# Optimization experiments

Measured on AMD Instinct MI355X. Metric: run time of the kernel, lower is better.

## Reference

```python
import jax, jax.numpy as jnp
import numpy as np

B, N, DIM, H, DH = 2, 2048, 512, 8, 64
INNER = H * DH  # == DIM, required by the q.view trick in the original module
STEP = 4


def setup_inputs() -> dict:
    key = jax.random.key(0)
    k1, k2, k3 = jax.random.split(key, 3)
    x = jax.random.normal(k1, (B, N, DIM), jnp.float32)
    # to_qkv: Linear(dim, 4*inner_dim, bias=False); stored as [in, out] for x @ W
    W_qkv = jax.random.normal(k2, (DIM, 4 * INNER), jnp.float32) * 0.02
    # to_out: Linear(2*inner_dim, dim) with bias
    W_out = jax.random.normal(k3, (2 * INNER, DIM), jnp.float32) * 0.02
    b_out = jnp.zeros((DIM,), jnp.float32)
    return {"x": x, "W_qkv": W_qkv, "W_out": W_out, "b_out": b_out}


def reference(x, W_qkv, W_out, b_out):
    b, n, _ = x.shape
    h, dh = H, DH
    scale = dh ** -0.5

    qkvt = x @ W_qkv                       # [b, n, 4*inner]
    q, k, v, t = jnp.split(qkvt, 4, axis=-1)
    to_heads = lambda z: z.reshape(b, n, h, dh).transpose(0, 2, 1, 3)  # [b,h,n,dh]
    q, k, v, t = map(to_heads, (q, k, v, t))

    # pad q by repeating its last row yushu times (note: yushu=4 when n%4==0)
    yushu = STEP - n % STEP
    q = jnp.concatenate([q, jnp.repeat(q[:, :, -1:, :], yushu, axis=2)], axis=2)
    q0 = q.reshape(b, h, STEP, (n + yushu) // STEP, dh)[:, :, 0]  # [b,h,(n+yushu)/4,dh]
    q = jnp.tile(q0, (1, 1, STEP, 1))[:, :, :n]                   # [b,h,n,dh]

    dots = jnp.einsum('bhnd,bhmd->bhnm', q, k) * scale
    attn1 = jax.nn.softmax(dots, axis=-1)

    # fixed distance-decay attention: exp(-|i-j|/e), column-normalized
    pos = jnp.arange(1, n + 1, dtype=x.dtype)
    tg = jnp.abs(pos[None, :] - pos[:, None])                     # [n, n]
    attn2 = jnp.exp(-tg / jnp.exp(jnp.asarray(1.0, x.dtype)))
    # torch: attn2 / attn2.sum(-1) broadcasts [n] over last axis (divides column j by row-sum j)
    attn2 = attn2 / attn2.sum(-1)

    out1 = jnp.einsum('bhnm,bhmd->bhnd', attn1, v)
    out2 = jnp.einsum('nm,bhmd->bhnd', attn2, t)  # attn2 shared across b,h; no repeat needed
    out = jnp.concatenate([out1, out2], axis=-1)   # [b,h,n,2*dh]
    out = out.transpose(0, 2, 1, 3).reshape(b, n, 2 * h * dh)  # b n (h d)
    return out @ W_out + b_out  # dropout=0.0 -> identity
```

## Files before the change

### kernel.cpp

```cpp
#include <hip/hip_runtime.h>

#define NSEQ 2048
#define NB   2
#define NH   8

typedef unsigned short u16;
typedef __attribute__((ext_vector_type(8))) short s8v;
typedef __attribute__((ext_vector_type(4))) float f4v;

static __device__ __forceinline__ u16 f2bf(float f) {
  unsigned u = __float_as_uint(f);
  unsigned r = (u + 0x7fffu + ((u >> 16) & 1u)) >> 16;
  return (u16)r;
}
static __device__ __forceinline__ unsigned pk2(float a, float b) {
  return (unsigned)f2bf(a) | ((unsigned)f2bf(b) << 16);
}
static __device__ __forceinline__ float bf2f(u16 v) {
  return __uint_as_float(((unsigned)v) << 16);
}

typedef __attribute__((address_space(3))) unsigned int lds_u32;
typedef const __attribute__((address_space(1))) unsigned int glob_u32;
static __device__ __forceinline__ void load16(const void* g, void* l) {
  __builtin_amdgcn_global_load_lds((glob_u32*)g, (lds_u32*)l, 16, 0, 0);
}

__global__ __launch_bounds__(256)
void prep_kernel(const float* __restrict__ x, const float* __restrict__ Wqkv,
                 const float* __restrict__ Wout, u16* __restrict__ xb,
                 u16* __restrict__ WqkvT, u16* __restrict__ W1hi,
                 u16* __restrict__ W2hi) {
  __shared__ float tile[32][33];
  const int bid = blockIdx.x;
  if (bid < 1024) {
    long i = ((long)bid * 256 + threadIdx.x) * 8;
    float4 a = *(const float4*)&x[i];
    float4 b = *(const float4*)&x[i + 4];
    uint4 w;
    w.x = pk2(a.x, a.y); w.y = pk2(a.z, a.w);
    w.z = pk2(b.x, b.y); w.w = pk2(b.z, b.w);
    *(uint4*)&xb[i] = w;
    return;
  }
  const int tx = threadIdx.x & 31, ty = threadIdx.x >> 5;
  if (bid < 2048) {
    int b2 = bid - 1024;
    int c0 = (b2 & 63) * 32, r0 = (b2 >> 6) * 32;
#pragma unroll
    for (int s = 0; s < 32; s += 8)
      tile[ty + s][tx] = Wqkv[(long)(r0 + ty + s) * 2048 + c0 + tx];
    __syncthreads();
#pragma unroll
    for (int s = 0; s < 32; s += 8)
      WqkvT[(long)(c0 + ty + s) * 512 + r0 + tx] = f2bf(tile[tx][ty + s]);
    return;
  }
  {
    int b3 = bid - 2048;
    int part = b3 >= 256;
    if (part) b3 -= 256;
    u16* hi = part ? W2hi : W1hi;
    int c0 = (b3 & 15) * 32, r0 = (b3 >> 4) * 32;
#pragma unroll
    for (int s = 0; s < 32; s += 8) {
      int k = r0 + ty + s;
      int srcrow = ((k >> 6) * 128) + part * 64 + (k & 63);
      tile[ty + s][tx] = Wout[(long)srcrow * 512 + c0 + tx];
    }
    __syncthreads();
#pragma unroll
    for (int s = 0; s < 32; s += 8) {
      long o = (long)(c0 + ty + s) * 512 + r0 + tx;
      hi[o] = f2bf(tile[tx][ty + s]);
    }
  }
}

__global__ __launch_bounds__(256)
void gemm1_fused(const u16* __restrict__ xb, const u16* __restrict__ WqkvT,
                 u16* __restrict__ qkvtb, u16* __restrict__ qu,
                 u16* __restrict__ VtG) {
  const int bx = blockIdx.x, by = blockIdx.y;
  const bool isq = bx >= 12;
  if (isq && by >= 9) return;
  __shared__ alignas(16) u16 As[128 * 32];
  __shared__ alignas(16) u16 Bs[128 * 32];
  const int tid = threadIdx.x, lane = tid & 63, wave = tid >> 6;
  const int l15 = lane & 15, quad = lane >> 4;
  const int wr = wave >> 1, wc = wave & 1;
  const int Brow0 = isq ? (bx - 12) * 128 : 512 + bx * 128;

  f4v acc[4][4];
#pragma unroll
  for (int i = 0; i < 4; ++i)
#pragma unroll
    for (int j = 0; j < 4; ++j) acc[i][j] = (f4v){0.f, 0.f, 0.f, 0.f};

  for (int k0 = 0; k0 < 512; k0 += 32) {
    __syncthreads();
#pragma unroll
    for (int c = 0; c < 2; ++c) {
      int off = (c * 4 + wave) * 1024 + lane * 16;
      int r = off >> 6, cb = (off & 63) >> 1;
      int gar;
      if (!isq) {
        gar = by * 128 + r;
      } else {
        int rr = by * 128 + r;
        int b = rr >= 576;
        int s = rr - (b ? 576 : 0);
        if (s >= 513) s -= 513;
        gar = b * 2048 + s;
      }
      load16(&xb[(long)gar * 512 + k0 + cb], ((char*)As) + off);
      load16(&WqkvT[(long)(Brow0 + r) * 512 + k0 + cb], ((char*)Bs) + off);
    }
    __syncthreads();

    s8v bf[4];
#pragma unroll
    for (int j = 0; j < 4; ++j)
      bf[j] = *(const s8v*)&Bs[(wc * 64 + j * 16 + l15) * 32 + quad * 8];
#pragma unroll
    for (int i = 0; i < 4; ++i) {
      s8v af = *(const s8v*)&As[(wr * 64 + i * 16 + l15) * 32 + quad * 8];
#pragma unroll
      for (int j = 0; j < 4; ++j)
        acc[i][j] = __builtin_amdgcn_mfma_f32_16x16x32_bf16(af, bf[j], acc[i][j], 0, 0, 0);
    }
  }

  const bool isv = (!isq) && bx >= 4 && bx < 8;
#pragma unroll
  for (int i = 0; i < 4; ++i) {
    int row0 = by * 128 + wr * 64 + i * 16 + quad * 4;
    if (isv) {
      int b = row0 >> 11, n = row0 & 2047;
#pragma unroll
      for (int j = 0; j < 4; ++j) {
        int vcol = (bx - 4) * 128 + wc * 64 + j * 16 + l15;
        int h = vcol >> 6, d = vcol & 63;
        uint2 w;
        w.x = pk2(acc[i][j][0], acc[i][j][1]);
        w.y = pk2(acc[i][j][2], acc[i][j][3]);
        *(uint2*)&VtG[(((long)b * 8 + h) * 64 + d) * 2048 + n] = w;
      }
    } else {
#pragma unroll
      for (int rr = 0; rr < 4; ++rr) {
        int row = row0 + rr;
#pragma unroll
        for (int j = 0; j < 4; ++j) {
          int col = wc * 64 + j * 16 + l15;
          u16 v = f2bf(acc[i][j][rr]);
          if (!isq)
            qkvtb[(long)row * 2048 + 512 + bx * 128 + col] = v;
          else
            qu[(long)row * 512 + (bx - 12) * 128 + col] = v;
        }
      }
    }
  }
}

template<int BM, int BN, int TI, int TJ, bool BSPLIT, bool BIAS, bool OUTBF, bool ADDG1>
__global__ __launch_bounds__(256)
void gemm_bt_bf16(const u16* __restrict__ A, const u16* __restrict__ Bhi,
                  const u16* __restrict__ Blo, const float* __restrict__ bias,
                  const float* __restrict__ G1, void* __restrict__ Cout,
                  int M, int N, int K) {
  __shared__ alignas(16) u16 As[BM * 32];
  __shared__ alignas(16) u16 Bs[BN * 32];
  __shared__ alignas(16) u16 Bs2[BSPLIT ? BN * 32 : 8];
  const int tid = threadIdx.x, lane = tid & 63, wave = tid >> 6;
  const int l15 = lane & 15, quad = lane >> 4;
  const int wr = wave >> 1, wc = wave & 1;
  const long m0 = (long)blockIdx.y * BM, n0 = (long)blockIdx.x * BN;

  f4v acc[TI][TJ];
#pragma unroll
  for (int i = 0; i < TI; ++i)
#pragma unroll
    for (int j = 0; j < TJ; ++j) acc[i][j] = (f4v){0.f, 0.f, 0.f, 0.f};

  for (int k0 = 0; k0 < K; k0 += 32) {
    __syncthreads();
#pragma unroll
    for (int c = 0; c < BM / 64; ++c) {
      int off = (c * 4 + wave) * 1024 + lane * 16;
      int r = off >> 6, cb = (off & 63) >> 1;
      load16(&A[(m0 + r) * K + k0 + cb], ((char*)As) + off);
    }
#pragma unroll
    for (int c = 0; c < BN / 64; ++c) {
      int off = (c * 4 + wave) * 1024 + lane * 16;
      int r = off >> 6, cb = (off & 63) >> 1;
      load16(&Bhi[(n0 + r) * K + k0 + cb], ((char*)Bs) + off);
      if constexpr (BSPLIT)
        load16(&Blo[(n0 + r) * K + k0 + cb], ((char*)Bs2) + off);
    }
    __syncthreads();

    s8v bf[TJ], bf2[BSPLIT ? TJ : 1];
#pragma unroll
    for (int j = 0; j < TJ; ++j) {
      bf[j] = *(const s8v*)&Bs[(wc * (TJ * 16) + j * 16 + l15) * 32 + quad * 8];
      if constexpr (BSPLIT)
        bf2[j] = *(const s8v*)&Bs2[(wc * (TJ * 16) + j * 16 + l15) * 32 + quad * 8];
    }
#pragma unroll
    for (int i = 0; i < TI; ++i) {
      s8v af = *(const s8v*)&As[(wr * (TI * 16) + i * 16 + l15) * 32 + quad * 8];
#pragma unroll
      for (int j = 0; j < TJ; ++j) {
        acc[i][j] = __builtin_amdgcn_mfma_f32_16x16x32_bf16(af, bf[j], acc[i][j], 0, 0, 0);
        if constexpr (BSPLIT)
          acc[i][j] = __builtin_amdgcn_mfma_f32_16x16x32_bf16(af, bf2[j], acc[i][j], 0, 0, 0);
      }
    }
  }

#pragma unroll
  for (int i = 0; i < TI; ++i)
#pragma unroll
    for (int rr = 0; rr < 4; ++rr) {
      long row = m0 + wr * (TI * 16) + i * 16 + quad * 4 + rr;
      long g1row = 0;
      if constexpr (ADDG1)
        g1row = (long)((int)(row >> 11) * 576 + ((int)(row & 2047) % 513)) * 512;
#pragma unroll
      for (int j = 0; j < TJ; ++j) {
        long col = n0 + wc * (TJ * 16) + j * 16 + l15;
        float v = acc[i][j][rr];
        if constexpr (BIAS) v += bias[col];
        if constexpr (ADDG1) v += G1[g1row + col];
        if constexpr (OUTBF)
          ((u16*)Cout)[row * N + col] = f2bf(v);
        else
          ((float*)Cout)[row * N + col] = v;
      }
    }
}

__global__ __launch_bounds__(256)
void attn_kernel(const u16* __restrict__ qkvt, const u16* __restrict__ qu,
                 const u16* __restrict__ VtG, float* __restrict__ Opart,
                 float* __restrict__ rspart) {
  __shared__ alignas(16) u16 Qs[64 * 64];
  __shared__ alignas(16) u16 Ks[64 * 64];
  __shared__ alignas(16) u16 Vt[64 * 64];
  __shared__ alignas(16) u16 Ps[4][16][72];

  const int tid  = threadIdx.x;
  const int lane = tid & 63, wave = tid >> 6;
  const int l15  = lane & 15, quad = lane >> 4;
  const int qtile = blockIdx.x;
  const int bh = blockIdx.y;
  const int split = blockIdx.z;
  const int b = bh >> 3, h = bh & 7;
  const long rowbase = (long)b * NSEQ;
  const long vtbase = ((long)b * 8 + h) * 64 * 2048;

  int srow[2], scs[2];
#pragma unroll
  for (int p = 0; p < 2; ++p) {
    int idx = p * 256 + tid;
    srow[p] = idx >> 3;
    scs[p] = (idx & 7) ^ (srow[p] & 7);
  }

#pragma unroll
  for (int p = 0; p < 2; ++p) {
    int v = qtile * 64 + srow[p];
    int eff = v >= 513 ? v - 513 : v;
    load16(&qu[((long)(b * 576 + eff)) * 512 + h * 64 + scs[p] * 8],
           (char*)Qs + (p * 256 + wave * 64) * 16);
  }
  __syncthreads();

  s8v qf[2];
  {
    const int mrow = wave * 16 + l15;
    const int c0 = quad ^ (mrow & 7);
    qf[0] = *(const s8v*)&Qs[mrow * 64 + c0 * 8];
    qf[1] = *(const s8v*)&Qs[mrow * 64 + (c0 ^ 4) * 8];
  }

  f4v oacc[4];
#pragma unroll
  for (int i = 0; i < 4; ++i) oacc[i] = (f4v){0.f, 0.f, 0.f, 0.f};
  float rs[4] = {0.f, 0.f, 0.f, 0.f};

  for (int kt = 0; kt < 8; ++kt) {
    __syncthreads();
    const int kb = split * 512 + kt * 64;
#pragma unroll
    for (int p = 0; p < 2; ++p) {
      load16(&qkvt[(rowbase + kb + srow[p]) * 2048 + 512 + h * 64 + scs[p] * 8],
             (char*)Ks + (p * 256 + wave * 64) * 16);
      load16(&VtG[vtbase + (long)srow[p] * 2048 + kb + scs[p] * 8],
             (char*)Vt + (p * 256 + wave * 64) * 16);
    }
    __syncthreads();

#pragma unroll
    for (int nt = 0; nt < 4; ++nt) {
      f4v s = {0.f, 0.f, 0.f, 0.f};
      const int kr = nt * 16 + l15;
      const int kc0 = quad ^ (kr & 7);
      s8v kf0 = *(const s8v*)&Ks[kr * 64 + kc0 * 8];
      s8v kf1 = *(const s8v*)&Ks[kr * 64 + (kc0 ^ 4) * 8];
      s = __builtin_amdgcn_mfma_f32_16x16x32_bf16(qf[0], kf0, s, 0, 0, 0);
      s = __builtin_amdgcn_mfma_f32_16x16x32_bf16(qf[1], kf1, s, 0, 0, 0);
#pragma unroll
      for (int rr = 0; rr < 4; ++rr) {
        float p = __expf(s[rr] * 0.125f);
        rs[rr] += p;
        Ps[wave][quad * 4 + rr][nt * 16 + l15] = f2bf(p);
      }
    }
    asm volatile("" ::: "memory");

    s8v pf0 = *(const s8v*)&Ps[wave][l15][quad * 8];
    s8v pf1 = *(const s8v*)&Ps[wave][l15][32 + quad * 8];
#pragma unroll
    for (int nt = 0; nt < 4; ++nt) {
      const int vr = nt * 16 + l15;
      const int vc0 = quad ^ (vr & 7);
      s8v vf0 = *(const s8v*)&Vt[vr * 64 + vc0 * 8];
      s8v vf1 = *(const s8v*)&Vt[vr * 64 + (vc0 ^ 4) * 8];
      oacc[nt] = __builtin_amdgcn_mfma_f32_16x16x32_bf16(pf0, vf0, oacc[nt], 0, 0, 0);
      oacc[nt] = __builtin_amdgcn_mfma_f32_16x16x32_bf16(pf1, vf1, oacc[nt], 0, 0, 0);
    }
  }

  const long sb = ((long)split * 16 + bh) * 576;
#pragma unroll
  for (int rr = 0; rr < 4; ++rr) {
    float t = rs[rr];
    t += __shfl_xor(t, 1);
    t += __shfl_xor(t, 2);
    t += __shfl_xor(t, 4);
    t += __shfl_xor(t, 8);
    int row = qtile * 64 + wave * 16 + quad * 4 + rr;
    if (l15 == 0) rspart[sb + row] = t;
#pragma unroll
    for (int nt = 0; nt < 4; ++nt)
      Opart[(sb + row) * 64 + nt * 16 + l15] = oacc[nt][rr];
  }
}

__global__ __launch_bounds__(256)
void post_kernel(const u16* __restrict__ qkvt, const float* __restrict__ Opart,
                 const float* __restrict__ rspart, u16* __restrict__ O1u,
                 u16* __restrict__ O2) {
  __shared__ u16 Ts[256 * 64];
  __shared__ float Is[256];
  const int tid = threadIdx.x;
  const int bid = blockIdx.x;
  if (bid >= 512) {
    int idx = (bid - 512) * 256 + tid;
    int d4 = idx & 15, rowbh = idx >> 4;
    int bh = rowbh / 576, row = rowbh - bh * 576;
    int b = bh >> 3, h = bh & 7;
    float4 o = {0.f, 0.f, 0.f, 0.f};
    float rsum = 0.f;
#pragma unroll
    for (int s = 0; s < 4; ++s) {
      long base = ((long)s * 16 + bh) * 576 + row;
      float4 v = *(const float4*)&Opart[base * 64 + d4 * 4];
      o.x += v.x; o.y += v.y; o.z += v.z; o.w += v.w;
      rsum += rspart[base];
    }
    float inv = 1.0f / rsum;
    uint2 w = {pk2(o.x * inv, o.y * inv), pk2(o.z * inv, o.w * inv)};
    *(uint2*)&O1u[((long)(b * 576 + row)) * 512 + h * 64 + d4 * 4] = w;
    return;
  }
  const int rg = bid & 31;
  const int bh = bid >> 5;
  const int b = bh >> 3, h = bh & 7;
  const int g0 = rg * 64 - 96;
#pragma unroll
  for (int c = 0; c < 8; ++c) {
    int chunk = c * 256 + tid;
    int row = chunk >> 3, cc = chunk & 7;
    int gr = g0 + row;
    uint4 w = {0u, 0u, 0u, 0u};
    if (gr >= 0 && gr < NSEQ)
      w = *(const uint4*)&qkvt[((long)(b * NSEQ + gr)) * 2048 + 1536 + h * 64 + cc * 8];
    *(uint4*)&Ts[row * 64 + cc * 8] = w;
  }
  {
    const float ie = 0.36787944117144233f;
    const float rr = 0.69220062755534635f;
    const float inv1mr = 1.0f / (1.0f - rr);
    int gr = g0 + tid;
    float val = 0.f;
    if (gr >= 0 && gr < NSEQ) {
      float rj = __expf(-ie * (float)gr);
      float rn = __expf(-ie * (float)(NSEQ - 1 - gr));
      float s = 1.0f + (rr - rr * rj) * inv1mr + (rr - rr * rn) * inv1mr;
      val = 1.0f / s;
    }
    Is[tid] = val;
  }
  __syncthreads();

  const int d = tid & 63, sub = tid >> 6;
  const float r = 0.69220062755534635f;
  const int lo = 96 + sub * 16;
  float F = 0.f;
  float Fv[16];
#pragma unroll 8
  for (int j = lo - 96; j < lo; ++j)
    F = F * r + Is[j] * bf2f(Ts[j * 64 + d]);
#pragma unroll
  for (int k = 0; k < 16; ++k) {
    int j = lo + k;
    F = F * r + Is[j] * bf2f(Ts[j * 64 + d]);
    Fv[k] = F;
  }
  float G = 0.f;
#pragma unroll 8
  for (int j = lo + 15 + 96; j > lo + 15; --j)
    G = G * r + Is[j] * bf2f(Ts[j * 64 + d]);
#pragma unroll
  for (int k = 15; k >= 0; --k) {
    int j = lo + k;
    float u = Is[j] * bf2f(Ts[j * 64 + d]);
    G = G * r + u;
    O2[((long)(b * NSEQ + g0 + j)) * 512 + h * 64 + d] = f2bf(Fv[k] + G - u);
  }
}

extern "C" void kernel_launch(void* const* d_in, const int* in_sizes, int n_in,
                              void* d_out, int out_size, void* d_ws, size_t ws_size,
                              hipStream_t stream) {
  (void)in_sizes; (void)n_in; (void)out_size; (void)ws_size;
  const float* x    = (const float*)d_in[0];
  const float* Wqkv = (const float*)d_in[1];
  const float* Wout = (const float*)d_in[2];
  const float* bout = (const float*)d_in[3];
  float* out = (float*)d_out;

  u16*   qkvtb = (u16*)d_ws;
  u16*   qu    = qkvtb + (size_t)4096 * 2048;
  u16*   VtG   = qu    + (size_t)1152 * 512;
  u16*   O2    = VtG   + (size_t)2 * 8 * 64 * 2048;
  u16*   O1u   = O2    + (size_t)4096 * 512;
  u16*   xb    = O1u   + (size_t)1152 * 512;
  u16*   WqkvT = xb    + (size_t)4096 * 512;
  u16*   W1hi  = WqkvT + (size_t)2048 * 512;
  u16*   W2hi  = W1hi  + (size_t)512 * 512;
  float* Opart = (float*)(W2hi + (size_t)512 * 512);
  float* rsp   = Opart + (size_t)4 * 16 * 576 * 64;
  float* G1    = Opart;

  prep_kernel<<<dim3(2560), 256, 0, stream>>>(x, Wqkv, Wout, xb, WqkvT, W1hi, W2hi);
  gemm1_fused<<<dim3(16, 32), 256, 0, stream>>>(xb, WqkvT, qkvtb, qu, VtG);
  attn_kernel<<<dim3(9, 16, 4), 256, 0, stream>>>(qkvtb, qu, VtG, Opart, rsp);
  post_kernel<<<dim3(1088), 256, 0, stream>>>(qkvtb, Opart, rsp, O1u, O2);
  gemm_bt_bf16<128, 64, 4, 2, false, false, false, false>
      <<<dim3(8, 9), 256, 0, stream>>>(O1u, W1hi, nullptr, nullptr, nullptr,
                                       G1, 1152, 512, 512);
  gemm_bt_bf16<128, 64, 4, 2, false, true, false, true>
      <<<dim3(8, 32), 256, 0, stream>>>(O2, W2hi, nullptr, bout, G1,
                                        out, 4096, 512, 512);
}
```

Before: 138.0 us.

## Merge two output projection GEMMs into one gathered K=1024 GEMM

Replaces the separate O1 projection GEMM (over compressed unique rows) plus the O2 GEMM with a G1 add by a single GEMM over K=1024. It concatenates the two weight halves and gathers O1u rows per output row while loading A. This removes one kernel launch and the fp32 G1 intermediate round-trip through memory. In exchange, the O1 projection is recomputed for all 4096 rows instead of 1152 unique rows, which increases MFMA work.

```diff
diff --git a/kernel.cpp b/kernel.cpp
--- a/kernel.cpp
+++ b/kernel.cpp
@@ -29,8 +29,7 @@
 __global__ __launch_bounds__(256)
 void prep_kernel(const float* __restrict__ x, const float* __restrict__ Wqkv,
                  const float* __restrict__ Wout, u16* __restrict__ xb,
-                 u16* __restrict__ WqkvT, u16* __restrict__ W1hi,
-                 u16* __restrict__ W2hi) {
+                 u16* __restrict__ WqkvT, u16* __restrict__ Wc) {
   __shared__ float tile[32][33];
   const int bid = blockIdx.x;
   if (bid < 1024) {
@@ -60,7 +59,6 @@
     int b3 = bid - 2048;
     int part = b3 >= 256;
     if (part) b3 -= 256;
-    u16* hi = part ? W2hi : W1hi;
     int c0 = (b3 & 15) * 32, r0 = (b3 >> 4) * 32;
 #pragma unroll
     for (int s = 0; s < 32; s += 8) {
@@ -69,10 +67,11 @@
       tile[ty + s][tx] = Wout[(long)srcrow * 512 + c0 + tx];
     }
     __syncthreads();
+    int koff = part ? 0 : 512;
 #pragma unroll
     for (int s = 0; s < 32; s += 8) {
-      long o = (long)(c0 + ty + s) * 512 + r0 + tx;
-      hi[o] = f2bf(tile[tx][ty + s]);
+      long o = (long)(c0 + ty + s) * 1024 + koff + r0 + tx;
+      Wc[o] = f2bf(tile[tx][ty + s]);
     }
   }
 }
@@ -164,81 +163,71 @@
   }
 }
 
-template<int BM, int BN, int TI, int TJ, bool BSPLIT, bool BIAS, bool OUTBF, bool ADDG1>
 __global__ __launch_bounds__(256)
-void gemm_bt_bf16(const u16* __restrict__ A, const u16* __restrict__ Bhi,
-                  const u16* __restrict__ Blo, const float* __restrict__ bias,
-                  const float* __restrict__ G1, void* __restrict__ Cout,
-                  int M, int N, int K) {
-  __shared__ alignas(16) u16 As[BM * 32];
-  __shared__ alignas(16) u16 Bs[BN * 32];
-  __shared__ alignas(16) u16 Bs2[BSPLIT ? BN * 32 : 8];
+void gemm2_merged(const u16* __restrict__ O2, const u16* __restrict__ O1u,
+                  const u16* __restrict__ Wc, const float* __restrict__ bias,
+                  float* __restrict__ C) {
+  __shared__ alignas(16) u16 As[128 * 32];
+  __shared__ alignas(16) u16 Bs[64 * 32];
   const int tid = threadIdx.x, lane = tid & 63, wave = tid >> 6;
   const int l15 = lane & 15, quad = lane >> 4;
   const int wr = wave >> 1, wc = wave & 1;
-  const long m0 = (long)blockIdx.y * BM, n0 = (long)blockIdx.x * BN;
-
-  f4v acc[TI][TJ];
-#pragma unroll
-  for (int i = 0; i < TI; ++i)
-#pragma unroll
-    for (int j = 0; j < TJ; ++j) acc[i][j] = (f4v){0.f, 0.f, 0.f, 0.f};
-
-  for (int k0 = 0; k0 < K; k0 += 32) {
-    __syncthreads();
-#pragma unroll
-    for (int c = 0; c < BM / 64; ++c) {
-      int off = (c * 4 + wave) * 1024 + lane * 16;
-      int r = off >> 6, cb = (off & 63) >> 1;
-      load16(&A[(m0 + r) * K + k0 + cb], ((char*)As) + off);
-    }
-#pragma unroll
-    for (int c = 0; c < BN / 64; ++c) {
-      int off = (c * 4 + wave) * 1024 + lane * 16;
-      int r = off >> 6, cb = (off & 63) >> 1;
-      load16(&Bhi[(n0 + r) * K + k0 + cb], ((char*)Bs) + off);
-      if constexpr (BSPLIT)
-        load16(&Blo[(n0 + r) * K + k0 + cb], ((char*)Bs2) + off);
-    }
-    __syncthreads();
-
-    s8v bf[TJ], bf2[BSPLIT ? TJ : 1];
-#pragma unroll
-    for (int j = 0; j < TJ; ++j) {
-      bf[j] = *(const s8v*)&Bs[(wc * (TJ * 16) + j * 16 + l15) * 32 + quad * 8];
-      if constexpr (BSPLIT)
-        bf2[j] = *(const s8v*)&Bs2[(wc * (TJ * 16) + j * 16 + l15) * 32 + quad * 8];
-    }
-#pragma unroll
-    for (int i = 0; i < TI; ++i) {
-      s8v af = *(const s8v*)&As[(wr * (TI * 16) + i * 16 + l15) * 32 + quad * 8];
-#pragma unroll
-      for (int j = 0; j < TJ; ++j) {
+  const long m0 = (long)blockIdx.y * 128, n0 = (long)blockIdx.x * 64;
+
+  long baseO2[2], baseO1[2];
+  int offA[2];
+#pragma unroll
+  for (int c = 0; c < 2; ++c) {
+    int off = (c * 4 + wave) * 1024 + lane * 16;
+    int r = off >> 6, cb = (off & 63) >> 1;
+    offA[c] = off;
+    long rowA = m0 + r;
+    int b = (int)(rowA >> 11);
+    int eff = (int)(rowA & 2047) % 513;
+    baseO2[c] = rowA * 512 + cb;
+    baseO1[c] = ((long)(b * 576 + eff)) * 512 + cb;
+  }
+  const int offB = wave * 1024 + lane * 16;
+  const long baseB = (long)(n0 + (offB >> 6)) * 1024 + ((offB & 63) >> 1);
+
+  f4v acc[4][2];
+#pragma unroll
+  for (int i = 0; i < 4; ++i)
+#pragma unroll
+    for (int j = 0; j < 2; ++j) acc[i][j] = (f4v){0.f, 0.f, 0.f, 0.f};
+
+  for (int k0 = 0; k0 < 1024; k0 += 32) {
+    __syncthreads();
+#pragma unroll
+    for (int c = 0; c < 2; ++c) {
+      const u16* src = (k0 < 512) ? &O2[baseO2[c] + k0] : &O1u[baseO1[c] + k0 - 512];
+      load16(src, ((char*)As) + offA[c]);
+    }
+    load16(&Wc[baseB + k0], ((char*)Bs) + offB);
+    __syncthreads();
+
+    s8v bf[2];
+#pragma unroll
+    for (int j = 0; j < 2; ++j)
+      bf[j] = *(const s8v*)&Bs[(wc * 32 + j * 16 + l15) * 32 + quad * 8];
+#pragma unroll
+    for (int i = 0; i < 4; ++i) {
+      s8v af = *(const s8v*)&As[(wr * 64 + i * 16 + l15) * 32 + quad * 8];
+#pragma unroll
+      for (int j = 0; j < 2; ++j)
         acc[i][j] = __builtin_amdgcn_mfma_f32_16x16x32_bf16(af, bf[j], acc[i][j], 0, 0, 0);
-        if constexpr (BSPLIT)
-          acc[i][j] = __builtin_amdgcn_mfma_f32_16x16x32_bf16(af, bf2[j], acc[i][j], 0, 0, 0);
-      }
-    }
-  }
-
-#pragma unroll
-  for (int i = 0; i < TI; ++i)
+    }
+  }
+
+#pragma unroll
+  for (int i = 0; i < 4; ++i)
 #pragma unroll
     for (int rr = 0; rr < 4; ++rr) {
-      long row = m0 + wr * (TI * 16) + i * 16 + quad * 4 + rr;
-      long g1row = 0;
-      if constexpr (ADDG1)
-        g1row = (long)((int)(row >> 11) * 576 + ((int)(row & 2047) % 513)) * 512;
-#pragma unroll
-      for (int j = 0; j < TJ; ++j) {
-        long col = n0 + wc * (TJ * 16) + j * 16 + l15;
-        float v = acc[i][j][rr];
-        if constexpr (BIAS) v += bias[col];
-        if constexpr (ADDG1) v += G1[g1row + col];
-        if constexpr (OUTBF)
-          ((u16*)Cout)[row * N + col] = f2bf(v);
-        else
-          ((float*)Cout)[row * N + col] = v;
+      long row = m0 + wr * 64 + i * 16 + quad * 4 + rr;
+#pragma unroll
+      for (int j = 0; j < 2; ++j) {
+        long col = n0 + wc * 32 + j * 16 + l15;
+        C[row * 512 + col] = acc[i][j][rr] + bias[col];
       }
     }
 }
@@ -452,20 +441,13 @@
   u16*   O1u   = O2    + (size_t)4096 * 512;
   u16*   xb    = O1u   + (size_t)1152 * 512;
   u16*   WqkvT = xb    + (size_t)4096 * 512;
-  u16*   W1hi  = WqkvT + (size_t)2048 * 512;
-  u16*   W2hi  = W1hi  + (size_t)512 * 512;
-  float* Opart = (float*)(W2hi + (size_t)512 * 512);
+  u16*   Wc    = WqkvT + (size_t)2048 * 512;
+  float* Opart = (float*)(Wc + (size_t)512 * 1024);
   float* rsp   = Opart + (size_t)4 * 16 * 576 * 64;
-  float* G1    = Opart;
-
-  prep_kernel<<<dim3(2560), 256, 0, stream>>>(x, Wqkv, Wout, xb, WqkvT, W1hi, W2hi);
+
+  prep_kernel<<<dim3(2560), 256, 0, stream>>>(x, Wqkv, Wout, xb, WqkvT, Wc);
   gemm1_fused<<<dim3(16, 32), 256, 0, stream>>>(xb, WqkvT, qkvtb, qu, VtG);
   attn_kernel<<<dim3(9, 16, 4), 256, 0, stream>>>(qkvtb, qu, VtG, Opart, rsp);
   post_kernel<<<dim3(1088), 256, 0, stream>>>(qkvtb, Opart, rsp, O1u, O2);
-  gemm_bt_bf16<128, 64, 4, 2, false, false, false, false>
-      <<<dim3(8, 9), 256, 0, stream>>>(O1u, W1hi, nullptr, nullptr, nullptr,
-                                       G1, 1152, 512, 512);
-  gemm_bt_bf16<128, 64, 4, 2, false, true, false, true>
-      <<<dim3(8, 32), 256, 0, stream>>>(O2, W2hi, nullptr, bout, G1,
-                                        out, 4096, 512, 512);
-}
+  gemm2_merged<<<dim3(8, 32), 256, 0, stream>>>(O2, O1u, Wc, bout, out);
+}
```

Result: faster. 132.9 us (-3.7%).
